# Performance work log

Hardware: AMD Instinct MI355X
Metric: run time of the kernel (lower is better)

Reference implementation:

```python
import jax, jax.numpy as jnp
import numpy as np

NUM, NUM_TOP, COBJ = 32, 32, 4   # num = MBS*ncobj, num_top, cobj_size = k//2
B, D, H = 300, 256, 256          # bag_size, feature dim, relation hidden
K_OBJ = 8                        # k (output cobj size)
FEA0 = 2 * NUM * COBJ            # orig_fea leading dim = MBS*K with K=2*ncobj*cobj_size


def setup_inputs() -> dict:
    key = jax.random.key(0)
    ks = jax.random.split(key, 8)
    return {
        "orig_fea": jax.random.normal(ks[0], (FEA0, B, D), dtype=jnp.float32),
        "ind0": jax.random.randint(ks[1], (NUM, NUM_TOP, COBJ), 0, B, dtype=jnp.int32),
        "ind1": jax.random.randint(ks[2], (NUM, NUM_TOP, COBJ), 0, B, dtype=jnp.int32),
        "k": K_OBJ,
        "W1a": jax.random.normal(ks[3], (D, H), dtype=jnp.float32) * (1.0 / np.sqrt(D)),
        "W1b": jax.random.normal(ks[4], (D, H), dtype=jnp.float32) * (1.0 / np.sqrt(D)),
        "b1": jnp.zeros((H,), dtype=jnp.float32),
        "W2": jax.random.normal(ks[5], (H, 1), dtype=jnp.float32) * (1.0 / np.sqrt(H)),
        "b2": jnp.zeros((1,), dtype=jnp.float32),
    }


def reference(orig_fea, ind0, ind1, k, W1a, W1b, b1, W2, b2):
    num, num_top, cobj = ind0.shape
    bag = orig_fea.shape[1]
    d = orig_fea.shape[2]
    # create_ids: stride bag_size over cobj positions -> [num, L], L = num_top*cobj
    off = (bag * jnp.arange(cobj, dtype=ind0.dtype))
    ids0 = (ind0 + off).reshape(num, -1)
    ids1 = (ind1 + off).reshape(num, -1)
    # rsolo_fea = reshape(orig_fea, [num, 2, pool, D]); pool = cobj*bag
    pool = (orig_fea.shape[0] * bag) // (2 * num)
    rsolo = orig_fea.reshape(num, 2, pool, d)
    # gather per-side features (dedup+inverse-gather in the original is an
    # optimization; direct gather yields the identical score matrix)
    f0 = jnp.take_along_axis(rsolo[:, 0], ids0[..., None], axis=1)  # [num, L, D]
    f1 = jnp.take_along_axis(rsolo[:, 1], ids1[..., None], axis=1)  # [num, L, D]
    # relation unit: score(a,b) = MLP(concat(f0_a, f1_b)) -> [num, L, L, 1]
    h0 = jnp.einsum('nad,dh->nah', f0, W1a)          # [num, L, H]
    h1 = jnp.einsum('nbd,dh->nbh', f1, W1b)          # [num, L, H]
    h = jax.nn.relu(h0[:, :, None, :] + h1[:, None, :, :] + b1)  # [num, L, L, H]
    scores = jnp.einsum('nabh,ho->nabo', h, W2) + b2              # [num, L, L, 1]
    # sum_kxk_patches with patch size k//2
    kp = k // 2
    L = num_top * cobj
    hk = L // kp
    scores = scores.reshape(num, hk, kp, hk, kp, 1).sum(axis=(2, 4))  # [num, m, l, 1]
    m = l = num_top
    scores = scores.reshape(num, m * l, 1)
    # get_pairs
    pairs = jnp.stack(jnp.meshgrid(jnp.arange(m, dtype=jnp.int32),
                                   jnp.arange(l, dtype=jnp.int32), indexing='ij'),
                      axis=-1).reshape(1, m * l, 2)
    pairs = jnp.broadcast_to(pairs, (num, m * l, 2))
    return scores, pairs
```

## Files before the change

kernel.cpp:

```cpp
#include <hip/hip_runtime.h>

#define NUMB 32
#define LL   128
#define POOL 1200
#define BAG  300
#define DD   256
#define HH   256
#define NS   (NUMB*32*32)

using bf16x8 = __bf16    __attribute__((ext_vector_type(8)));
using f32x4  = float     __attribute__((ext_vector_type(4)));
using fp16x2 = __fp16    __attribute__((ext_vector_type(2)));
using h16x2  = _Float16  __attribute__((ext_vector_type(2)));
using h16x8  = _Float16  __attribute__((ext_vector_type(8)));

typedef const __attribute__((address_space(1))) unsigned int* gas_t;
typedef       __attribute__((address_space(3))) unsigned int* las_t;

static __device__ __forceinline__ unsigned short f2bf(float x) {
    unsigned u = __float_as_uint(x);
    return (unsigned short)((u + 0x7FFFu + ((u >> 16) & 1u)) >> 16);
}

static __device__ __forceinline__ float pkh(float a, float b) {
    fp16x2 p = __builtin_amdgcn_cvt_pkrtz(a, b);
    return __builtin_bit_cast(float, p);
}

static __device__ __forceinline__ unsigned int pkbf(float a, float b) {
    unsigned int r;
    asm("v_cvt_pk_bf16_f32 %0, %1, %2" : "=v"(r) : "v"(a), "v"(b));
    return r;
}

__global__ __launch_bounds__(256) void k_prep(
    const float* __restrict__ W1a, const float* __restrict__ W1b,
    unsigned short* __restrict__ WtP)
{
    const int blk = blockIdx.x, t = threadIdx.x;
    const int side = blk >> 4, kc = blk & 15;
    const float* W = side ? W1b : W1a;
    __shared__ float T[16][257];
    const int row = t >> 4, c = t & 15;
#pragma unroll
    for (int i = 0; i < 4; ++i) {
        int col4 = c + i * 16;
        float4 v = *(const float4*)(W + (size_t)(kc * 16 + row) * HH + col4 * 4);
        T[row][col4 * 4 + 0] = v.x; T[row][col4 * 4 + 1] = v.y;
        T[row][col4 * 4 + 2] = v.z; T[row][col4 * 4 + 3] = v.w;
    }
    __syncthreads();
    const int n = t, ht = n >> 6, nn = n & 63;
#pragma unroll
    for (int j = 0; j < 2; ++j) {
        unsigned short tmp[8] __attribute__((aligned(16)));
#pragma unroll
        for (int e = 0; e < 8; ++e) tmp[e] = f2bf(T[j * 8 + e][n]);
        int U = kc * 2 + j;
        int pos = U ^ (nn & 7);
        size_t unit = ((size_t)((side * 4 + ht) * 64 + nn)) * 32 + pos;
        *(float4*)(WtP + unit * 8) = *(float4*)tmp;
    }
}

__global__ __launch_bounds__(256) void k_gemm(
    const float* __restrict__ fea,
    const int*   __restrict__ ind0,
    const int*   __restrict__ ind1,
    const float* __restrict__ b1,
    const unsigned short* __restrict__ WtP,
    unsigned short* __restrict__ Hh)
{
    __shared__ unsigned short As[64 * 256] __attribute__((aligned(16)));
    __shared__ unsigned short Bs[64 * 256] __attribute__((aligned(16)));

    const int b0 = blockIdx.x;
    const int b = (b0 & 7) * 64 + (b0 >> 3);
    const int ht = b & 3, rt = b >> 2;
    const int side = rt >> 6;
    const int R0 = rt * 64;
    const int t = threadIdx.x, w = t >> 6, lane = t & 63;

    const unsigned short* Wbase = WtP + ((size_t)(side * 4 + ht)) * 64 * 256;
#pragma unroll
    for (int i = 0; i < 8; ++i) {
        int chunk = w * 8 + i;
        __builtin_amdgcn_global_load_lds(
            (gas_t)(const void*)(Wbase + chunk * 512 + lane * 8),
            (las_t)(void*)(As + chunk * 512),
            16, 0, 0);
    }

    {
        const int lr = t >> 2;
        const int g = R0 + lr;
        const int rs = g & 4095, n_ = rs >> 7, a_ = rs & 127;
        const int id = (side ? ind1 : ind0)[n_ * LL + a_] + BAG * (a_ & 3);
        const float* arow = fea + (size_t)((n_ * 2 + side) * POOL + id) * DD;
        const int sw = lr & 7;
#pragma unroll
        for (int j0 = 0; j0 < 8; ++j0) {
            int u = j0 * 4 + (t & 3);
            float4 v0 = *(const float4*)(arow + u * 8);
            float4 v1 = *(const float4*)(arow + u * 8 + 4);
            unsigned int tmp[4] __attribute__((aligned(16)));
            tmp[0] = pkbf(v0.x, v0.y);
            tmp[1] = pkbf(v0.z, v0.w);
            tmp[2] = pkbf(v1.x, v1.y);
            tmp[3] = pkbf(v1.z, v1.w);
            int pos = u ^ sw;
            *(f32x4*)&Bs[lr * 256 + pos * 8] = *(const f32x4*)tmp;
        }
    }
    __syncthreads();

    const int l15 = lane & 15, q = lane >> 4;
    const int wh = w >> 1, wr = w & 1;
    f32x4 acc[2][2] = {};
#pragma unroll
    for (int kk = 0; kk < 8; ++kk) {
        const int u = kk * 4 + q;
        bf16x8 af[2], bfv[2];
#pragma unroll
        for (int a = 0; a < 2; ++a) {
            int hr = wh * 32 + a * 16 + l15;
            af[a] = *(const bf16x8*)&As[hr * 256 + (u ^ (hr & 7)) * 8];
        }
#pragma unroll
        for (int r = 0; r < 2; ++r) {
            int rr = wr * 32 + r * 16 + l15;
            bfv[r] = *(const bf16x8*)&Bs[rr * 256 + (u ^ (rr & 7)) * 8];
        }
#pragma unroll
        for (int a = 0; a < 2; ++a)
#pragma unroll
            for (int r = 0; r < 2; ++r)
                acc[a][r] = __builtin_amdgcn_mfma_f32_16x16x32_bf16(af[a], bfv[r], acc[a][r], 0, 0, 0);
    }

    const int hq = ht * 64 + wh * 32 + q * 4;
    float4 bias[2];
    bias[0] = make_float4(0.f, 0.f, 0.f, 0.f);
    bias[1] = bias[0];
    if (side == 0) {
        bias[0] = *(const float4*)(b1 + hq);
        bias[1] = *(const float4*)(b1 + hq + 16);
    }
#pragma unroll
    for (int a = 0; a < 2; ++a)
#pragma unroll
    for (int r = 0; r < 2; ++r) {
        int frow = R0 + wr * 32 + r * 16 + l15;
        float2 pk;
        pk.x = pkh(acc[a][r][0] + bias[a].x, acc[a][r][1] + bias[a].y);
        pk.y = pkh(acc[a][r][2] + bias[a].z, acc[a][r][3] + bias[a].w);
        *(float2*)&Hh[(size_t)frow * HH + hq + a * 16] = pk;
    }
}

__global__ __launch_bounds__(256) void k_pair(
    const unsigned short* __restrict__ Hh,
    const float* __restrict__ W2,
    const float* __restrict__ b2,
    float*       __restrict__ out)
{
    __shared__ unsigned short s0[32 * 256] __attribute__((aligned(16)));
    __shared__ unsigned short s1[32 * 256] __attribute__((aligned(16)));
    __shared__ unsigned short w2s[256]     __attribute__((aligned(16)));
    __shared__ float sred[256];

    const int b0 = blockIdx.x;
    int b = (b0 & 7) * 64 + (b0 >> 3);
    const int jt = b & 3;  b >>= 2;
    const int it = b & 3;  b >>= 2;
    const int n  = b;
    const int t = threadIdx.x, w = t >> 6, lane = t & 63;

    const size_t base0 = ((size_t)(n * LL) + it * 32) * HH;
    const size_t base1 = ((size_t)(NUMB * LL + n * LL) + jt * 32) * HH;

    {
        const int pos = lane & 31, rhalf = lane >> 5;
#pragma unroll
        for (int i = 0; i < 4; ++i) {
            int rowbase = w * 8 + i * 2;
            int row = rowbase + rhalf;
            int f = pos ^ ((row >> 2) & 7);
            __builtin_amdgcn_global_load_lds(
                (gas_t)(const void*)(Hh + base0 + (size_t)row * HH + f * 8),
                (las_t)(void*)(s0 + rowbase * 256), 16, 0, 0);
            __builtin_amdgcn_global_load_lds(
                (gas_t)(const void*)(Hh + base1 + (size_t)row * HH + f * 8),
                (las_t)(void*)(s1 + rowbase * 256), 16, 0, 0);
        }
    }
    if (t < 64) {
        float4 v = *(const float4*)(W2 + t * 4);
        float2 pk;
        pk.x = pkh(v.x, v.y);
        pk.y = pkh(v.z, v.w);
        *(float2*)&w2s[t * 4] = pk;
    }
    __syncthreads();

    const int il = (t >> 3) & 7, jl = t & 7;
    float acc[4][4] = {{0.f,0.f,0.f,0.f},{0.f,0.f,0.f,0.f},
                       {0.f,0.f,0.f,0.f},{0.f,0.f,0.f,0.f}};

#pragma unroll
    for (int f = 0; f < 8; ++f) {
        h16x8 wv = *(const h16x8*)&w2s[(w * 8 + f) * 8];
        const h16x2* wp = (const h16x2*)&wv;
        h16x8 av[4], bv[4];
#pragma unroll
        for (int r = 0; r < 4; ++r)
            av[r] = *(const h16x8*)&s0[(il * 4 + r) * 256 + (w * 8 + (f ^ il)) * 8];
#pragma unroll
        for (int s = 0; s < 4; ++s)
            bv[s] = *(const h16x8*)&s1[(jl * 4 + s) * 256 + (w * 8 + (f ^ jl)) * 8];
        const h16x8 zero = {0, 0, 0, 0, 0, 0, 0, 0};
#pragma unroll
        for (int r = 0; r < 4; ++r)
#pragma unroll
            for (int s = 0; s < 4; ++s) {
                h16x8 sum = av[r] + bv[s];
                sum = __builtin_elementwise_max(sum, zero);
                const h16x2* sp = (const h16x2*)&sum;
#pragma unroll
                for (int u = 0; u < 4; ++u)
                    acc[r][s] = __builtin_amdgcn_fdot2(sp[u], wp[u], acc[r][s], false);
            }
    }

    float total = 0.f;
#pragma unroll
    for (int r = 0; r < 4; ++r)
#pragma unroll
        for (int s = 0; s < 4; ++s) total += acc[r][s];

    sred[t] = total;
    __syncthreads();

    if (t < 64) {
        float sum = sred[t] + sred[t + 64] + sred[t + 128] + sred[t + 192]
                  + 16.0f * b2[0];
        int i = it * 8 + (t >> 3);
        int j = jt * 8 + (t & 7);
        int p = n * 1024 + i * 32 + j;
        out[p] = sum;
        *(float2*)(out + NS + 2 * p) = make_float2((float)i, (float)j);
    }
}

extern "C" void kernel_launch(void* const* d_in, const int* in_sizes, int n_in,
                              void* d_out, int out_size, void* d_ws, size_t ws_size,
                              hipStream_t stream)
{
    const float* fea  = (const float*)d_in[0];
    const int*   ind0 = (const int*)  d_in[1];
    const int*   ind1 = (const int*)  d_in[2];
    const float* W1a  = (const float*)d_in[4];
    const float* W1b  = (const float*)d_in[5];
    const float* b1   = (const float*)d_in[6];
    const float* W2   = (const float*)d_in[7];
    const float* b2   = (const float*)d_in[8];
    float* out = (float*)d_out;

    unsigned short* WtP = (unsigned short*)d_ws;
    unsigned short* Hh  = (unsigned short*)((char*)d_ws + 512 * 1024);

    hipLaunchKernelGGL(k_prep, dim3(32), dim3(256), 0, stream,
                       W1a, W1b, WtP);
    hipLaunchKernelGGL(k_gemm, dim3(512), dim3(256), 0, stream,
                       fea, ind0, ind1, b1, WtP, Hh);
    hipLaunchKernelGGL(k_pair, dim3(512), dim3(256), 0, stream,
                       Hh, W2, b2, out);
}
```

Before: 129.6 us.

## Fuse prep, GEMM and pair kernels into one cooperative kernel with grid syncs

Merges the weight-prep, gather+GEMM, and pairwise relation kernels into a single cooperative launch. Two grid-wide barriers replace the kernel boundaries. The feature gather and bf16 conversion now overlaps with the weight-prep blocks before the first barrier. The aim is to remove two kernel launch gaps and tail effects. The cost is grid-sync overhead, plus a requirement that all 512 blocks are co-resident. If the cooperative launch fails, the code falls back to the original three launches.

```diff
diff --git a/kernel.cpp b/kernel.cpp
--- a/kernel.cpp
+++ b/kernel.cpp
@@ -1,4 +1,7 @@
 #include <hip/hip_runtime.h>
+#include <hip/hip_cooperative_groups.h>
+
+namespace cg = cooperative_groups;
 
 #define NUMB 32
 #define LL   128
@@ -31,6 +34,224 @@
     unsigned int r;
     asm("v_cvt_pk_bf16_f32 %0, %1, %2" : "=v"(r) : "v"(a), "v"(b));
     return r;
+}
+
+__global__ __launch_bounds__(256) void k_fused(
+    const float* __restrict__ fea,
+    const int*   __restrict__ ind0,
+    const int*   __restrict__ ind1,
+    const float* __restrict__ W1a,
+    const float* __restrict__ W1b,
+    const float* __restrict__ b1,
+    const float* __restrict__ W2,
+    const float* __restrict__ b2,
+    unsigned short* __restrict__ WtP,
+    unsigned short* __restrict__ Hh,
+    float*       __restrict__ out)
+{
+    __shared__ unsigned short As[64 * 256] __attribute__((aligned(16)));
+    __shared__ unsigned short Bs[64 * 256] __attribute__((aligned(16)));
+
+    const int b0 = blockIdx.x;
+    const int t = threadIdx.x, w = t >> 6, lane = t & 63;
+
+    const int bg = (b0 & 7) * 64 + (b0 >> 3);
+    const int ht = bg & 3, rt = bg >> 2;
+    const int side = rt >> 6;
+    const int R0 = rt * 64;
+
+    if (b0 < 32) {
+        const int pside = b0 >> 4, kc = b0 & 15;
+        const float* W = pside ? W1b : W1a;
+        float (*T)[257] = (float (*)[257])(void*)As;
+        const int row = t >> 4, c = t & 15;
+#pragma unroll
+        for (int i = 0; i < 4; ++i) {
+            int col4 = c + i * 16;
+            float4 v = *(const float4*)(W + (size_t)(kc * 16 + row) * HH + col4 * 4);
+            T[row][col4 * 4 + 0] = v.x; T[row][col4 * 4 + 1] = v.y;
+            T[row][col4 * 4 + 2] = v.z; T[row][col4 * 4 + 3] = v.w;
+        }
+        __syncthreads();
+        const int pht = t >> 6, nn = t & 63;
+#pragma unroll
+        for (int j = 0; j < 2; ++j) {
+            unsigned short tmp[8] __attribute__((aligned(16)));
+#pragma unroll
+            for (int e = 0; e < 8; ++e) tmp[e] = f2bf(T[j * 8 + e][t]);
+            int U = kc * 2 + j;
+            int pos = U ^ (nn & 7);
+            size_t unit = ((size_t)((pside * 4 + pht) * 64 + nn)) * 32 + pos;
+            *(float4*)(WtP + unit * 8) = *(float4*)tmp;
+        }
+        __syncthreads();
+    }
+
+    {
+        const int lr = t >> 2;
+        const int g = R0 + lr;
+        const int rs = g & 4095, n_ = rs >> 7, a_ = rs & 127;
+        const int id = (side ? ind1 : ind0)[n_ * LL + a_] + BAG * (a_ & 3);
+        const float* arow = fea + (size_t)((n_ * 2 + side) * POOL + id) * DD;
+        const int sw = lr & 7;
+#pragma unroll
+        for (int j0 = 0; j0 < 8; ++j0) {
+            int u = j0 * 4 + (t & 3);
+            float4 v0 = *(const float4*)(arow + u * 8);
+            float4 v1 = *(const float4*)(arow + u * 8 + 4);
+            unsigned int tmp[4] __attribute__((aligned(16)));
+            tmp[0] = pkbf(v0.x, v0.y);
+            tmp[1] = pkbf(v0.z, v0.w);
+            tmp[2] = pkbf(v1.x, v1.y);
+            tmp[3] = pkbf(v1.z, v1.w);
+            int pos = u ^ sw;
+            *(f32x4*)&Bs[lr * 256 + pos * 8] = *(const f32x4*)tmp;
+        }
+    }
+    __syncthreads();
+    cg::this_grid().sync();
+
+    const unsigned short* Wbase = WtP + ((size_t)(side * 4 + ht)) * 64 * 256;
+#pragma unroll
+    for (int i = 0; i < 8; ++i) {
+        int chunk = w * 8 + i;
+        __builtin_amdgcn_global_load_lds(
+            (gas_t)(const void*)(Wbase + chunk * 512 + lane * 8),
+            (las_t)(void*)(As + chunk * 512),
+            16, 0, 0);
+    }
+    __syncthreads();
+
+    const int l15 = lane & 15, q = lane >> 4;
+    const int wh = w >> 1, wr = w & 1;
+    f32x4 acc[2][2] = {};
+#pragma unroll
+    for (int kk = 0; kk < 8; ++kk) {
+        const int u = kk * 4 + q;
+        bf16x8 af[2], bfv[2];
+#pragma unroll
+        for (int a = 0; a < 2; ++a) {
+            int hr = wh * 32 + a * 16 + l15;
+            af[a] = *(const bf16x8*)&As[hr * 256 + (u ^ (hr & 7)) * 8];
+        }
+#pragma unroll
+        for (int r = 0; r < 2; ++r) {
+            int rr = wr * 32 + r * 16 + l15;
+            bfv[r] = *(const bf16x8*)&Bs[rr * 256 + (u ^ (rr & 7)) * 8];
+        }
+#pragma unroll
+        for (int a = 0; a < 2; ++a)
+#pragma unroll
+            for (int r = 0; r < 2; ++r)
+                acc[a][r] = __builtin_amdgcn_mfma_f32_16x16x32_bf16(af[a], bfv[r], acc[a][r], 0, 0, 0);
+    }
+
+    {
+        const int hq = ht * 64 + wh * 32 + q * 4;
+        float4 bias[2];
+        bias[0] = make_float4(0.f, 0.f, 0.f, 0.f);
+        bias[1] = bias[0];
+        if (side == 0) {
+            bias[0] = *(const float4*)(b1 + hq);
+            bias[1] = *(const float4*)(b1 + hq + 16);
+        }
+#pragma unroll
+        for (int a = 0; a < 2; ++a)
+#pragma unroll
+        for (int r = 0; r < 2; ++r) {
+            int frow = R0 + wr * 32 + r * 16 + l15;
+            float2 pk;
+            pk.x = pkh(acc[a][r][0] + bias[a].x, acc[a][r][1] + bias[a].y);
+            pk.y = pkh(acc[a][r][2] + bias[a].z, acc[a][r][3] + bias[a].w);
+            *(float2*)&Hh[(size_t)frow * HH + hq + a * 16] = pk;
+        }
+    }
+    cg::this_grid().sync();
+
+    unsigned short* s0  = As;
+    unsigned short* s1  = As + 32 * 256;
+    unsigned short* w2s = Bs;
+    float*          sred = (float*)(void*)(Bs + 256);
+
+    int bp = (b0 & 7) * 64 + (b0 >> 3);
+    const int jt = bp & 3;  bp >>= 2;
+    const int it = bp & 3;  bp >>= 2;
+    const int n  = bp;
+
+    const size_t base0 = ((size_t)(n * LL) + it * 32) * HH;
+    const size_t base1 = ((size_t)(NUMB * LL + n * LL) + jt * 32) * HH;
+
+    {
+        const int pos = lane & 31, rhalf = lane >> 5;
+#pragma unroll
+        for (int i = 0; i < 4; ++i) {
+            int rowbase = w * 8 + i * 2;
+            int row = rowbase + rhalf;
+            int f = pos ^ ((row >> 2) & 7);
+            __builtin_amdgcn_global_load_lds(
+                (gas_t)(const void*)(Hh + base0 + (size_t)row * HH + f * 8),
+                (las_t)(void*)(s0 + rowbase * 256), 16, 0, 0);
+            __builtin_amdgcn_global_load_lds(
+                (gas_t)(const void*)(Hh + base1 + (size_t)row * HH + f * 8),
+                (las_t)(void*)(s1 + rowbase * 256), 16, 0, 0);
+        }
+    }
+    if (t < 64) {
+        float4 v = *(const float4*)(W2 + t * 4);
+        float2 pk;
+        pk.x = pkh(v.x, v.y);
+        pk.y = pkh(v.z, v.w);
+        *(float2*)&w2s[t * 4] = pk;
+    }
+    __syncthreads();
+
+    const int il = (t >> 3) & 7, jl = t & 7;
+    float acc2[4][4] = {{0.f,0.f,0.f,0.f},{0.f,0.f,0.f,0.f},
+                        {0.f,0.f,0.f,0.f},{0.f,0.f,0.f,0.f}};
+
+#pragma unroll
+    for (int f = 0; f < 8; ++f) {
+        h16x8 wv = *(const h16x8*)&w2s[(w * 8 + f) * 8];
+        const h16x2* wp = (const h16x2*)&wv;
+        h16x8 av[4], bv[4];
+#pragma unroll
+        for (int r = 0; r < 4; ++r)
+            av[r] = *(const h16x8*)&s0[(il * 4 + r) * 256 + (w * 8 + (f ^ il)) * 8];
+#pragma unroll
+        for (int s = 0; s < 4; ++s)
+            bv[s] = *(const h16x8*)&s1[(jl * 4 + s) * 256 + (w * 8 + (f ^ jl)) * 8];
+        const h16x8 zero = {0, 0, 0, 0, 0, 0, 0, 0};
+#pragma unroll
+        for (int r = 0; r < 4; ++r)
+#pragma unroll
+            for (int s = 0; s < 4; ++s) {
+                h16x8 sum = av[r] + bv[s];
+                sum = __builtin_elementwise_max(sum, zero);
+                const h16x2* sp = (const h16x2*)&sum;
+#pragma unroll
+                for (int u = 0; u < 4; ++u)
+                    acc2[r][s] = __builtin_amdgcn_fdot2(sp[u], wp[u], acc2[r][s], false);
+            }
+    }
+
+    float total = 0.f;
+#pragma unroll
+    for (int r = 0; r < 4; ++r)
+#pragma unroll
+        for (int s = 0; s < 4; ++s) total += acc2[r][s];
+
+    sred[t] = total;
+    __syncthreads();
+
+    if (t < 64) {
+        float sum = sred[t] + sred[t + 64] + sred[t + 128] + sred[t + 192]
+                  + 16.0f * b2[0];
+        int i = it * 8 + (t >> 3);
+        int j = jt * 8 + (t & 7);
+        int p = n * 1024 + i * 32 + j;
+        out[p] = sum;
+        *(float2*)(out + NS + 2 * p) = make_float2((float)i, (float)j);
+    }
 }
 
 __global__ __launch_bounds__(256) void k_prep(
@@ -50,12 +271,12 @@
         T[row][col4 * 4 + 2] = v.z; T[row][col4 * 4 + 3] = v.w;
     }
     __syncthreads();
-    const int n = t, ht = n >> 6, nn = n & 63;
+    const int ht = t >> 6, nn = t & 63;
 #pragma unroll
     for (int j = 0; j < 2; ++j) {
         unsigned short tmp[8] __attribute__((aligned(16)));
 #pragma unroll
-        for (int e = 0; e < 8; ++e) tmp[e] = f2bf(T[j * 8 + e][n]);
+        for (int e = 0; e < 8; ++e) tmp[e] = f2bf(T[j * 8 + e][t]);
         int U = kc * 2 + j;
         int pos = U ^ (nn & 7);
         size_t unit = ((size_t)((side * 4 + ht) * 64 + nn)) * 32 + pos;
@@ -90,7 +311,6 @@
             (las_t)(void*)(As + chunk * 512),
             16, 0, 0);
     }
-
     {
         const int lr = t >> 2;
         const int g = R0 + lr;
@@ -269,10 +489,20 @@
     unsigned short* WtP = (unsigned short*)d_ws;
     unsigned short* Hh  = (unsigned short*)((char*)d_ws + 512 * 1024);
 
-    hipLaunchKernelGGL(k_prep, dim3(32), dim3(256), 0, stream,
-                       W1a, W1b, WtP);
-    hipLaunchKernelGGL(k_gemm, dim3(512), dim3(256), 0, stream,
-                       fea, ind0, ind1, b1, WtP, Hh);
-    hipLaunchKernelGGL(k_pair, dim3(512), dim3(256), 0, stream,
-                       Hh, W2, b2, out);
-}
+    void* kargs[] = {
+        (void*)&fea, (void*)&ind0, (void*)&ind1,
+        (void*)&W1a, (void*)&W1b, (void*)&b1,
+        (void*)&W2,  (void*)&b2,
+        (void*)&WtP, (void*)&Hh, (void*)&out
+    };
+    hipError_t e = hipLaunchCooperativeKernel(k_fused, dim3(512), dim3(256),
+                                              kargs, 0u, stream);
+    if (e != hipSuccess) {
+        hipLaunchKernelGGL(k_prep, dim3(32), dim3(256), 0, stream,
+                           W1a, W1b, WtP);
+        hipLaunchKernelGGL(k_gemm, dim3(512), dim3(256), 0, stream,
+                           fea, ind0, ind1, b1, WtP, Hh);
+        hipLaunchKernelGGL(k_pair, dim3(512), dim3(256), 0, stream,
+                           Hh, W2, b2, out);
+    }
+}
```

Result: slower. 258.5 us (+99.4%).
